# Kernel tuning notes

Measured on AMD Instinct MI355X. Metric: run time of the kernel, lower is better.

The kernel has to match this reference:

```python
import jax, jax.numpy as jnp
import numpy as np
import math

N = 100000
E = 1600000
D = 256          # input_size
H = 64           # head_size = input_size // n_heads = 256 // 4


def setup_inputs() -> dict:
    key = jax.random.key(0)
    k1, k2, k3, k4, k5 = jax.random.split(key, 5)
    X = jax.random.normal(k1, (N, D), dtype=jnp.float32)
    edge_index = jax.random.randint(k2, (2, E), 0, N, dtype=jnp.int64)
    # Linear(input_size, head_size, bias=False) weights, stored as [D, H] so Q = X @ Wq
    s = 1.0 / math.sqrt(D)
    Wq = jax.random.uniform(k3, (D, H), dtype=jnp.float32, minval=-s, maxval=s)
    Wk = jax.random.uniform(k4, (D, H), dtype=jnp.float32, minval=-s, maxval=s)
    Wv = jax.random.uniform(k5, (D, H), dtype=jnp.float32, minval=-s, maxval=s)
    return {"X": X, "Wq": Wq, "Wk": Wk, "Wv": Wv, "edge_index": edge_index}


def reference(X, Wq, Wk, Wv, edge_index):
    dk = math.sqrt(H)
    Q = X @ Wq  # [N, H]
    K = X @ Wk
    V = X @ Wv
    src = edge_index[0]  # row of sparse matrix -> softmax segment (dim=1 softmax)
    dst = edge_index[1]  # column -> neighbor supplying K/V
    scores = jnp.sum(Q[src] * K[dst], axis=-1) / dk  # [E]
    # per-row (per src node) stable softmax over edges
    m = jax.ops.segment_max(scores, src, num_segments=N)          # [N], -inf for empty rows
    m = jnp.where(jnp.isfinite(m), m, 0.0)
    e = jnp.exp(scores - m[src])                                   # [E]
    denom = jax.ops.segment_sum(e, src, num_segments=N)            # [N]
    alpha = e / jnp.maximum(denom[src], 1e-38)                     # [E]
    # scatter-weighted V aggregation: out[i] = sum_{(i,j) in edges} alpha_ij * V[j]
    out = jax.ops.segment_sum(alpha[:, None] * V[dst], src, num_segments=N)  # [N, H]
    return out
```

## Files before the change

### kernel.cpp

```cpp
#include <hip/hip_runtime.h>

typedef unsigned short u16;
typedef unsigned int u32;
typedef short short8 __attribute__((ext_vector_type(8)));
typedef float f32x4 __attribute__((ext_vector_type(4)));
typedef u32 u32x4 __attribute__((ext_vector_type(4)));

__device__ __forceinline__ u16 f2bf(float f) {
    union { float f; u32 i; } c; c.f = f;
    u32 i = c.i;
    return (u16)((i + 0x7FFFu + ((i >> 16) & 1u)) >> 16);
}
__device__ __forceinline__ float bf2f(u16 u) {
    union { u32 i; float f; } c; c.i = ((u32)u) << 16; return c.f;
}
__device__ __forceinline__ void bf2x(u32 p, float& lo, float& hi) {
    union { u32 i; float f; } a, b;
    a.i = p << 16; b.i = p & 0xFFFF0000u;
    lo = a.f; hi = b.f;
}
__device__ __forceinline__ u32 cvtpk_bf16(float lo, float hi) {
    u32 r;
    asm("v_cvt_pk_bf16_f32 %0, %1, %2" : "=v"(r) : "v"(lo), "v"(hi));
    return r;
}

__global__ void wfrag_kernel(const float* __restrict__ Wq,
                             const float* __restrict__ Wk,
                             const float* __restrict__ Wv,
                             u16* __restrict__ wf)
{
    int idx = blockIdx.x * 256 + threadIdx.x;
    if (idx >= 12 * 8 * 64) return;
    int lane = idx & 63;
    int s = (idx >> 6) & 7;
    int t = idx >> 9;
    int n = t * 16 + (lane & 15);
    const float* Wsrc = (n < 64) ? Wq : ((n < 128) ? Wk : Wv);
    int col = n & 63;
    int kbase = s * 32 + (lane >> 4) * 8;
    u16 o[8];
#pragma unroll
    for (int j = 0; j < 8; ++j) o[j] = f2bf(Wsrc[(size_t)(kbase + j) * 64 + col]);
    *(short8*)(wf + (size_t)idx * 8) = *(const short8*)o;
}

#define TM 32
__global__ __launch_bounds__(256, 2) void qkv_mfma(
    const float* __restrict__ X, const u16* __restrict__ wf,
    float* __restrict__ Qs, u16* __restrict__ KVsb,
    int N, int NT)
{
    __shared__ float xs[TM * 256];

    const int tid  = threadIdx.x;
    const int lane = tid & 63;
    const int wave = tid >> 6;
    const int m    = lane & 15;
    const int quad = lane >> 4;
    const int t0   = wave * 3;

    const short8* wfp = (const short8*)wf;
    short8 bfr0[8], bfr1[8], bfr2[8];
#pragma unroll
    for (int s = 0; s < 8; ++s) {
        bfr0[s] = wfp[(size_t)((t0 + 0) * 8 + s) * 64 + lane];
        bfr1[s] = wfp[(size_t)((t0 + 1) * 8 + s) * 64 + lane];
        bfr2[s] = wfp[(size_t)((t0 + 2) * 8 + s) * 64 + lane];
    }

    for (int tile = blockIdx.x; tile < NT; tile += gridDim.x) {
#pragma unroll
        for (int it = 0; it < 8; ++it) {
            int c0  = (it * 4 + wave) * 64;
            int c   = c0 + lane;
            int row = c >> 6;
            int sblk = (c & 63) ^ (row & 7);
            int arow = tile * TM + row;
            if (arow >= N) arow = N - 1;
            const float* g = X + (size_t)arow * 256 + sblk * 4;
            float* l = xs + c0 * 4;
            __builtin_amdgcn_global_load_lds(
                (const __attribute__((address_space(1))) void*)g,
                (__attribute__((address_space(3))) void*)l, 16, 0, 0);
        }
        __syncthreads();

        f32x4 acc[2][3];
#pragma unroll
        for (int rb = 0; rb < 2; ++rb)
#pragma unroll
            for (int tt = 0; tt < 3; ++tt) acc[rb][tt] = (f32x4)0.f;

#pragma unroll
        for (int rb = 0; rb < 2; ++rb) {
            const int row = rb * 16 + m;
            const float* xrow = xs + row * 256;
            const int sw = m & 7;
#pragma unroll
            for (int s = 0; s < 8; ++s) {
                int B0 = quad * 2 + s * 8;
                float4 a0 = *(const float4*)(xrow + ((B0)     ^ sw) * 4);
                float4 a1 = *(const float4*)(xrow + ((B0 + 1) ^ sw) * 4);
                union { u32x4 u; short8 s8; } af;
                af.u.x = cvtpk_bf16(a0.x, a0.y);
                af.u.y = cvtpk_bf16(a0.z, a0.w);
                af.u.z = cvtpk_bf16(a1.x, a1.y);
                af.u.w = cvtpk_bf16(a1.z, a1.w);
                acc[rb][0] = __builtin_amdgcn_mfma_f32_16x16x32_bf16(af.s8, bfr0[s], acc[rb][0], 0, 0, 0);
                acc[rb][1] = __builtin_amdgcn_mfma_f32_16x16x32_bf16(af.s8, bfr1[s], acc[rb][1], 0, 0, 0);
                acc[rb][2] = __builtin_amdgcn_mfma_f32_16x16x32_bf16(af.s8, bfr2[s], acc[rb][2], 0, 0, 0);
            }
        }

#pragma unroll
        for (int rb = 0; rb < 2; ++rb) {
            int rbase = tile * TM + rb * 16 + quad * 4;
#pragma unroll
            for (int tt = 0; tt < 3; ++tt) {
                int t = t0 + tt;
                int col = (t & 3) * 16 + m;
#pragma unroll
                for (int r = 0; r < 4; ++r) {
                    int rr = rbase + r;
                    if (rr >= N) continue;
                    float v = acc[rb][tt][r];
                    if (t < 4)      Qs  [(size_t)rr * 64  + col]      = v;
                    else if (t < 8) KVsb[(size_t)rr * 128 + col]      = f2bf(v);
                    else            KVsb[(size_t)rr * 128 + 64 + col] = f2bf(v);
                }
            }
        }
        __syncthreads();
    }
}


__global__ __launch_bounds__(256) void count_kernel(
    const int* __restrict__ src, int* __restrict__ bsize,
    int E, int N, int NB, int chunk)
{
    __shared__ int cnt[512];
    for (int i = threadIdx.x; i < 512; i += 256) cnt[i] = 0;
    __syncthreads();
    int lo = blockIdx.x * chunk;
    int hi = min(E, lo + chunk);
    for (int e = lo + (int)threadIdx.x; e < hi; e += 256) {
        int s = src[e];
        if ((unsigned)s < (unsigned)N) atomicAdd(&cnt[s >> 8], 1);
    }
    __syncthreads();
    for (int b = threadIdx.x; b < NB; b += 256)
        if (cnt[b]) atomicAdd(&bsize[b], cnt[b]);
}

__global__ __launch_bounds__(512) void scan391_kernel(
    const int* __restrict__ bsize, int* __restrict__ bbase,
    int* __restrict__ cursor, int* __restrict__ row_ptr_N, int NB)
{
    __shared__ int sd[512];
    int t = threadIdx.x;
    int v = (t < NB) ? bsize[t] : 0;
    sd[t] = v;
    __syncthreads();
    for (int off = 1; off < 512; off <<= 1) {
        int x = (t >= off) ? sd[t - off] : 0;
        __syncthreads();
        sd[t] += x;
        __syncthreads();
    }
    if (t < NB) {
        int excl = sd[t] - v;
        bbase[t] = excl;
        cursor[t] = excl;
        if (t == NB - 1) {
            bbase[NB] = sd[t];
            *row_ptr_N = sd[t];
        }
    }
}

__global__ __launch_bounds__(256) void scatter_pairs_kernel(
    const int* __restrict__ src, const int* __restrict__ dst,
    int* __restrict__ cursor, int2* __restrict__ pairs,
    int E, int N, int NB, int chunk)
{
    __shared__ int cnt[512];
    __shared__ int basei[512];
    for (int i = threadIdx.x; i < 512; i += 256) cnt[i] = 0;
    __syncthreads();
    int lo = blockIdx.x * chunk;
    int hi = min(E, lo + chunk);
    for (int e = lo + (int)threadIdx.x; e < hi; e += 256) {
        int s = src[e];
        if ((unsigned)s < (unsigned)N) atomicAdd(&cnt[s >> 8], 1);
    }
    __syncthreads();
    for (int b = threadIdx.x; b < NB; b += 256)
        basei[b] = cnt[b] ? atomicAdd(&cursor[b], cnt[b]) : 0;
    __syncthreads();
    for (int i = threadIdx.x; i < 512; i += 256) cnt[i] = 0;
    __syncthreads();
    for (int e = lo + (int)threadIdx.x; e < hi; e += 256) {
        int s = src[e];
        if ((unsigned)s >= (unsigned)N) continue;
        int d = dst[e];
        if ((unsigned)d >= (unsigned)N) d = 0;
        int bk = s >> 8;
        int p = basei[bk] + atomicAdd(&cnt[bk], 1);
        pairs[p] = make_int2(s, d);
    }
}

#define MAXB 6144
__global__ __launch_bounds__(256) void sort_bucket_kernel(
    const int2* __restrict__ pairs, const int* __restrict__ bbase,
    int* __restrict__ row_ptr, int* __restrict__ sorted_dst, int N)
{
    __shared__ int deg[256];
    __shared__ int off[256];
    __shared__ int cur[256];
    __shared__ int ldst[MAXB];

    int bk = blockIdx.x;
    int n0 = bk * 256;
    int nn = min(256, N - n0);
    int base = bbase[bk];
    int size = bbase[bk + 1] - base;
    int t = threadIdx.x;

    deg[t] = 0;
    __syncthreads();
    for (int i = t; i < size; i += 256)
        atomicAdd(&deg[pairs[base + i].x & 255], 1);
    __syncthreads();
    off[t] = deg[t];
    __syncthreads();
    for (int s = 1; s < 256; s <<= 1) {
        int x = (t >= s) ? off[t - s] : 0;
        __syncthreads();
        off[t] += x;
        __syncthreads();
    }
    int excl = off[t] - deg[t];
    cur[t] = excl;
    if (t < nn) row_ptr[n0 + t] = base + excl;
    __syncthreads();
    int cap = min(size, MAXB);
    for (int i = t; i < size; i += 256) {
        int2 pr = pairs[base + i];
        int p = atomicAdd(&cur[pr.x & 255], 1);
        if (p < MAXB) ldst[p] = pr.y;
    }
    __syncthreads();
    for (int i = t; i < cap; i += 256)
        sorted_dst[base + i] = ldst[i];
    for (int i = cap + t; i < size; i += 256)
        sorted_dst[base + i] = 0;
}

__global__ __launch_bounds__(256) void attn_csr(
    const float* __restrict__ Qs, const u16* __restrict__ KVsb,
    const int* __restrict__ row_ptr, const int* __restrict__ sdst,
    float* __restrict__ out, int N)
{
    int sg = (int)((blockIdx.x * 256 + threadIdx.x) >> 3);
    if (sg >= N) return;
    int sl = threadIdx.x & 7;

    const float* qp = Qs + (size_t)sg * 64 + sl * 8;
    float4 q0 = *(const float4*)(qp);
    float4 q1 = *(const float4*)(qp + 4);

    int beg = row_ptr[sg];
    int end = row_ptr[sg + 1];

    float l = 0.f;
    float a0 = 0.f, a1 = 0.f, a2 = 0.f, a3 = 0.f;
    float a4 = 0.f, a5 = 0.f, a6 = 0.f, a7 = 0.f;

    if (beg < end) {
        const int last = end - 1;
        uint4 kr[4], vr[4];
        int pd[4];

#pragma unroll
        for (int i = 0; i < 4; ++i) {
            int e = beg + i;
            int d = sdst[e <= last ? e : last];
            const u16* kv = KVsb + (size_t)d * 128 + sl * 8;
            kr[i] = *(const uint4*)(kv);
            vr[i] = *(const uint4*)(kv + 64);
            int ep = beg + 4 + i;
            pd[i] = sdst[ep <= last ? ep : last];
        }

        for (int base = beg; base < end; base += 4) {
#pragma unroll
            for (int i = 0; i < 4; ++i) {
                int e = base + i;
                uint4 k = kr[i], v = vr[i];

                {
                    const u16* kv = KVsb + (size_t)pd[i] * 128 + sl * 8;
                    kr[i] = *(const uint4*)(kv);
                    vr[i] = *(const uint4*)(kv + 64);
                    int ep = e + 8;
                    pd[i] = sdst[ep <= last ? ep : last];
                }

                float k0, k1, k2, k3, k4, k5, k6, k7;
                bf2x(k.x, k0, k1); bf2x(k.y, k2, k3);
                bf2x(k.z, k4, k5); bf2x(k.w, k6, k7);

                float p = q0.x * k0 + q0.y * k1 + q0.z * k2 + q0.w * k3
                        + q1.x * k4 + q1.y * k5 + q1.z * k6 + q1.w * k7;
                p += __shfl_xor(p, 1);
                p += __shfl_xor(p, 2);
                p += __shfl_xor(p, 4);

                float pe = __expf(p * 0.125f);

                float v0, v1, v2, v3, v4, v5, v6, v7;
                bf2x(v.x, v0, v1); bf2x(v.y, v2, v3);
                bf2x(v.z, v4, v5); bf2x(v.w, v6, v7);

                if (e < end) {
                    l += pe;
                    a0 += pe * v0; a1 += pe * v1; a2 += pe * v2; a3 += pe * v3;
                    a4 += pe * v4; a5 += pe * v5; a6 += pe * v6; a7 += pe * v7;
                }
            }
        }
    }

    float inv = (l > 0.f) ? (1.f / l) : 0.f;
    float* op = out + (size_t)sg * 64 + sl * 8;
    *(float4*)(op)     = make_float4(a0 * inv, a1 * inv, a2 * inv, a3 * inv);
    *(float4*)(op + 4) = make_float4(a4 * inv, a5 * inv, a6 * inv, a7 * inv);
}

extern "C" void kernel_launch(void* const* d_in, const int* in_sizes, int n_in,
                              void* d_out, int out_size, void* d_ws, size_t ws_size,
                              hipStream_t stream)
{
    const float* X  = (const float*)d_in[0];
    const float* Wq = (const float*)d_in[1];
    const float* Wk = (const float*)d_in[2];
    const float* Wv = (const float*)d_in[3];
    const int*   ei = (const int*)d_in[4];

    const int N = in_sizes[0] / 256;
    const int E = in_sizes[4] / 2;
    const int* src = ei;
    const int* dst = ei + E;
    const int NB = (N + 255) >> 8;

    char* w = (char*)d_ws;
    float* Qs = (float*)w;      w += (size_t)N * 64 * sizeof(float);
    u16* KVsb = (u16*)w;        w += (size_t)N * 128 * sizeof(u16);
    int2* pairs = (int2*)w;     w += (size_t)E * sizeof(int2);
    int* sorted_dst = (int*)w;  w += (size_t)E * sizeof(int);
    int* row_ptr = (int*)w;     w += (size_t)(N + 1) * sizeof(int);
    int* bsize = (int*)w;       w += (size_t)(NB + 1) * sizeof(int);
    int* bbase = (int*)w;       w += (size_t)(NB + 1) * sizeof(int);
    int* cursor = (int*)w;      w += (size_t)(NB + 1) * sizeof(int);
    u16* wf = (u16*)w;          w += (size_t)12 * 8 * 64 * 8 * sizeof(u16);

    hipMemsetAsync(bsize, 0, (size_t)(NB + 1) * sizeof(int), stream);

    const int B1 = 160;
    const int chunk = (E + B1 - 1) / B1;
    const int NT = (N + TM - 1) / TM;

    wfrag_kernel<<<24, 256, 0, stream>>>(Wq, Wk, Wv, wf);
    qkv_mfma<<<768, 256, 0, stream>>>(X, wf, Qs, KVsb, N, NT);

    count_kernel<<<B1, 256, 0, stream>>>(src, bsize, E, N, NB, chunk);
    scan391_kernel<<<1, 512, 0, stream>>>(bsize, bbase, cursor, row_ptr + N, NB);
    scatter_pairs_kernel<<<B1, 256, 0, stream>>>(src, dst, cursor, pairs, E, N, NB, chunk);
    sort_bucket_kernel<<<NB, 256, 0, stream>>>(pairs, bbase, row_ptr, sorted_dst, N);

    attn_csr<<<(N * 8 + 255) / 256, 256, 0, stream>>>(
        Qs, KVsb, row_ptr, sorted_dst, (float*)d_out, N);
}
```

Before: 330.4 us.

## Use per-block bucket offsets, pack edge pairs into 32 bits, deepen gather prefetch

The global-atomic bucket cursor and the memset are replaced by a per-block count matrix that a single-block scan turns into deterministic per-block write offsets. Edge pairs are packed into one 32-bit word (24-bit dst, 8-bit local src), which halves the pairs traffic. The count/scatter grid grows to 320 blocks. The attention gather prefetch goes from 4 to 8 edges in flight. The serial scan over 320 rows in one block adds latency, the deeper prefetch raises register pressure, and the packing assumes N fits in 24 bits.

```diff
diff --git a/kernel.cpp b/kernel.cpp
--- a/kernel.cpp
+++ b/kernel.cpp
@@ -136,8 +136,10 @@
 }
 
 
+#define CB 320
+
 __global__ __launch_bounds__(256) void count_kernel(
-    const int* __restrict__ src, int* __restrict__ bsize,
+    const int* __restrict__ src, int* __restrict__ bcnt,
     int E, int N, int NB, int chunk)
 {
     __shared__ int cnt[512];
@@ -150,18 +152,25 @@
         if ((unsigned)s < (unsigned)N) atomicAdd(&cnt[s >> 8], 1);
     }
     __syncthreads();
-    for (int b = threadIdx.x; b < NB; b += 256)
-        if (cnt[b]) atomicAdd(&bsize[b], cnt[b]);
-}
-
-__global__ __launch_bounds__(512) void scan391_kernel(
-    const int* __restrict__ bsize, int* __restrict__ bbase,
-    int* __restrict__ cursor, int* __restrict__ row_ptr_N, int NB)
+    int* row = bcnt + (size_t)blockIdx.x * NB;
+    for (int b = threadIdx.x; b < NB; b += 256) row[b] = cnt[b];
+}
+
+__global__ __launch_bounds__(512) void scan_kernel(
+    const int* __restrict__ bcnt, int* __restrict__ blockbase,
+    int* __restrict__ bbase, int* __restrict__ row_ptr_N, int NB)
 {
     __shared__ int sd[512];
     int t = threadIdx.x;
-    int v = (t < NB) ? bsize[t] : 0;
-    sd[t] = v;
+    int run = 0;
+    if (t < NB) {
+        for (int blk = 0; blk < CB; ++blk) {
+            int v = bcnt[(size_t)blk * NB + t];
+            blockbase[(size_t)blk * NB + t] = run;
+            run += v;
+        }
+    }
+    sd[t] = (t < NB) ? run : 0;
     __syncthreads();
     for (int off = 1; off < 512; off <<= 1) {
         int x = (t >= off) ? sd[t - off] : 0;
@@ -170,9 +179,7 @@
         __syncthreads();
     }
     if (t < NB) {
-        int excl = sd[t] - v;
-        bbase[t] = excl;
-        cursor[t] = excl;
+        bbase[t] = sd[t] - run;
         if (t == NB - 1) {
             bbase[NB] = sd[t];
             *row_ptr_N = sd[t];
@@ -182,8 +189,8 @@
 
 __global__ __launch_bounds__(256) void scatter_pairs_kernel(
     const int* __restrict__ src, const int* __restrict__ dst,
-    int* __restrict__ cursor, int2* __restrict__ pairs,
-    int E, int N, int NB, int chunk)
+    const int* __restrict__ bbase, const int* __restrict__ blockbase,
+    u32* __restrict__ pairs, int E, int N, int NB, int chunk)
 {
     __shared__ int cnt[512];
     __shared__ int basei[512];
@@ -196,8 +203,9 @@
         if ((unsigned)s < (unsigned)N) atomicAdd(&cnt[s >> 8], 1);
     }
     __syncthreads();
+    const int* bb = blockbase + (size_t)blockIdx.x * NB;
     for (int b = threadIdx.x; b < NB; b += 256)
-        basei[b] = cnt[b] ? atomicAdd(&cursor[b], cnt[b]) : 0;
+        basei[b] = bbase[b] + bb[b];
     __syncthreads();
     for (int i = threadIdx.x; i < 512; i += 256) cnt[i] = 0;
     __syncthreads();
@@ -208,13 +216,13 @@
         if ((unsigned)d >= (unsigned)N) d = 0;
         int bk = s >> 8;
         int p = basei[bk] + atomicAdd(&cnt[bk], 1);
-        pairs[p] = make_int2(s, d);
+        pairs[p] = (u32)d | ((u32)(s & 255) << 24);
     }
 }
 
 #define MAXB 6144
 __global__ __launch_bounds__(256) void sort_bucket_kernel(
-    const int2* __restrict__ pairs, const int* __restrict__ bbase,
+    const u32* __restrict__ pairs, const int* __restrict__ bbase,
     int* __restrict__ row_ptr, int* __restrict__ sorted_dst, int N)
 {
     __shared__ int deg[256];
@@ -232,7 +240,7 @@
     deg[t] = 0;
     __syncthreads();
     for (int i = t; i < size; i += 256)
-        atomicAdd(&deg[pairs[base + i].x & 255], 1);
+        atomicAdd(&deg[pairs[base + i] >> 24], 1);
     __syncthreads();
     off[t] = deg[t];
     __syncthreads();
@@ -248,9 +256,9 @@
     __syncthreads();
     int cap = min(size, MAXB);
     for (int i = t; i < size; i += 256) {
-        int2 pr = pairs[base + i];
-        int p = atomicAdd(&cur[pr.x & 255], 1);
-        if (p < MAXB) ldst[p] = pr.y;
+        u32 pr = pairs[base + i];
+        int p = atomicAdd(&cur[pr >> 24], 1);
+        if (p < MAXB) ldst[p] = (int)(pr & 0xFFFFFFu);
     }
     __syncthreads();
     for (int i = t; i < cap; i += 256)
@@ -281,23 +289,23 @@
 
     if (beg < end) {
         const int last = end - 1;
-        uint4 kr[4], vr[4];
-        int pd[4];
-
-#pragma unroll
-        for (int i = 0; i < 4; ++i) {
+        uint4 kr[8], vr[8];
+        int pd[8];
+
+#pragma unroll
+        for (int i = 0; i < 8; ++i) {
             int e = beg + i;
             int d = sdst[e <= last ? e : last];
             const u16* kv = KVsb + (size_t)d * 128 + sl * 8;
             kr[i] = *(const uint4*)(kv);
             vr[i] = *(const uint4*)(kv + 64);
-            int ep = beg + 4 + i;
+            int ep = beg + 8 + i;
             pd[i] = sdst[ep <= last ? ep : last];
         }
 
-        for (int base = beg; base < end; base += 4) {
-#pragma unroll
-            for (int i = 0; i < 4; ++i) {
+        for (int base = beg; base < end; base += 8) {
+#pragma unroll
+            for (int i = 0; i < 8; ++i) {
                 int e = base + i;
                 uint4 k = kr[i], v = vr[i];
 
@@ -305,7 +313,7 @@
                     const u16* kv = KVsb + (size_t)pd[i] * 128 + sl * 8;
                     kr[i] = *(const uint4*)(kv);
                     vr[i] = *(const uint4*)(kv + 64);
-                    int ep = e + 8;
+                    int ep = e + 16;
                     pd[i] = sdst[ep <= last ? ep : last];
                 }
 
@@ -359,26 +367,24 @@
     char* w = (char*)d_ws;
     float* Qs = (float*)w;      w += (size_t)N * 64 * sizeof(float);
     u16* KVsb = (u16*)w;        w += (size_t)N * 128 * sizeof(u16);
-    int2* pairs = (int2*)w;     w += (size_t)E * sizeof(int2);
+    u32* pairs = (u32*)w;       w += (size_t)E * sizeof(u32);
     int* sorted_dst = (int*)w;  w += (size_t)E * sizeof(int);
     int* row_ptr = (int*)w;     w += (size_t)(N + 1) * sizeof(int);
-    int* bsize = (int*)w;       w += (size_t)(NB + 1) * sizeof(int);
     int* bbase = (int*)w;       w += (size_t)(NB + 1) * sizeof(int);
-    int* cursor = (int*)w;      w += (size_t)(NB + 1) * sizeof(int);
+    int* bcnt = (int*)w;        w += (size_t)CB * NB * sizeof(int);
+    int* blockbase = (int*)w;   w += (size_t)CB * NB * sizeof(int);
     u16* wf = (u16*)w;          w += (size_t)12 * 8 * 64 * 8 * sizeof(u16);
 
-    hipMemsetAsync(bsize, 0, (size_t)(NB + 1) * sizeof(int), stream);
-
-    const int B1 = 160;
-    const int chunk = (E + B1 - 1) / B1;
+    const int chunk = (E + CB - 1) / CB;
     const int NT = (N + TM - 1) / TM;
 
     wfrag_kernel<<<24, 256, 0, stream>>>(Wq, Wk, Wv, wf);
     qkv_mfma<<<768, 256, 0, stream>>>(X, wf, Qs, KVsb, N, NT);
 
-    count_kernel<<<B1, 256, 0, stream>>>(src, bsize, E, N, NB, chunk);
-    scan391_kernel<<<1, 512, 0, stream>>>(bsize, bbase, cursor, row_ptr + N, NB);
-    scatter_pairs_kernel<<<B1, 256, 0, stream>>>(src, dst, cursor, pairs, E, N, NB, chunk);
+    count_kernel<<<CB, 256, 0, stream>>>(src, bcnt, E, N, NB, chunk);
+    scan_kernel<<<1, 512, 0, stream>>>(bcnt, blockbase, bbase, row_ptr + N, NB);
+    scatter_pairs_kernel<<<CB, 256, 0, stream>>>(
+        src, dst, bbase, blockbase, pairs, E, N, NB, chunk);
     sort_bucket_kernel<<<NB, 256, 0, stream>>>(pairs, bbase, row_ptr, sorted_dst, N);
 
     attn_csr<<<(N * 8 + 255) / 256, 256, 0, stream>>>(
```

Measured after the change: 324.7 us. Within noise of the previous version (-1.7%).
